# Kernel optimization log

Measured on AMD Instinct MI355X. Metric: run time of the kernel, lower is better.

Reference implementation:

```python
import jax, jax.numpy as jnp
import numpy as np

H, W, C, B = 64, 64, 512, 16

def _dwconv(x, w, b, k):
    # x: [B,C,H,W]; w: [C,1,k,k] depthwise kernel; b: [C]
    pad = k // 2
    out = jax.lax.conv_general_dilated(
        x, w, window_strides=(1, 1), padding=[(pad, pad), (pad, pad)],
        dimension_numbers=('NCHW', 'OIHW', 'NCHW'), feature_group_count=x.shape[1])
    return out + b[None, :, None, None]

def setup_inputs() -> dict:
    key = jax.random.key(0)
    ks = jax.random.split(key, 7)
    x = jax.random.normal(ks[0], (B, 1 + H * W, C), dtype=jnp.float32)
    def kinit(k, ksize):
        fan_in = ksize * ksize  # groups=C -> in_ch per group = 1
        bound = 1.0 / np.sqrt(fan_in)
        return jax.random.uniform(k, (C, 1, ksize, ksize), jnp.float32, -bound, bound)
    w7 = kinit(ks[1], 7); b7 = jax.random.uniform(ks[2], (C,), jnp.float32, -1/7.0, 1/7.0)
    w5 = kinit(ks[3], 5); b5 = jax.random.uniform(ks[4], (C,), jnp.float32, -1/5.0, 1/5.0)
    w3 = kinit(ks[5], 3); b3 = jax.random.uniform(ks[6], (C,), jnp.float32, -1/3.0, 1/3.0)
    return {'x': x, 'w7': w7, 'b7': b7, 'w5': w5, 'b5': b5, 'w3': w3, 'b3': b3}

def reference(x, w7, b7, w5, b5, w3, b3):
    Bn, N, Cn = x.shape
    cls_token = x[:, 0]          # [B, C]
    feat_token = x[:, 1:]        # [B, H*W, C]
    cnn_feat = feat_token.transpose(0, 2, 1).reshape(Bn, Cn, H, W)
    y = (_dwconv(cnn_feat, w7, b7, 7) + cnn_feat
         + _dwconv(cnn_feat, w5, b5, 5)
         + _dwconv(cnn_feat, w3, b3, 3))
    y = y.reshape(Bn, Cn, H * W).transpose(0, 2, 1)   # [B, HW, C]
    return jnp.concatenate([cls_token[:, None, :], y], axis=1)
```

## Files before the change

kernel.cpp:

```cpp
#include <hip/hip_runtime.h>

#define Hh 64
#define Ww 64
#define Cc 512
#define Bb 16
#define NTOK (1 + Hh * Ww)
#define TW 8
#define TH 4

typedef float v2f __attribute__((ext_vector_type(2)));

__global__ void ppeg_prep(const float* __restrict__ w7, const float* __restrict__ b7,
                          const float* __restrict__ w5, const float* __restrict__ b5,
                          const float* __restrict__ w3, const float* __restrict__ b3,
                          const float* __restrict__ x, float* __restrict__ wt,
                          float* __restrict__ beff, float* __restrict__ out) {
    int idx = blockIdx.x * blockDim.x + threadIdx.x;
    if (idx < Cc * 49) {
        int c = idx / 49, t = idx % 49;
        int r = t / 7, s = t % 7;
        float v = w7[idx];
        if (r >= 1 && r <= 5 && s >= 1 && s <= 5) v += w5[c * 25 + (r - 1) * 5 + (s - 1)];
        if (r >= 2 && r <= 4 && s >= 2 && s <= 4) v += w3[c * 9 + (r - 2) * 3 + (s - 2)];
        if (t == 24) v += 1.0f;
        wt[t * Cc + c] = v;
    }
    if (idx < Cc) beff[idx] = b7[idx] + b5[idx] + b3[idx];
    if (idx < Bb * Cc) {
        int b = idx / Cc, c = idx % Cc;
        size_t o = (size_t)b * NTOK * Cc + c;
        out[o] = x[o];
    }
}

__global__ __launch_bounds__(256, 2)
void ppeg_conv(const float* __restrict__ x, const float* __restrict__ wt,
               const float* __restrict__ beff, float* __restrict__ out) {
    const int tx = threadIdx.x;
    const int ty = threadIdx.y;

    const int L     = blockIdx.x + 32 * (blockIdx.y + 4 * blockIdx.z);
    const int g_lin = (L & 7) * 256 + (L >> 3);
    const int sp    = g_lin & 31;
    const int g     = g_lin >> 5;
    const int cb    = (g & 3) * 128;
    const int b     = g >> 2;

    const int c0 = cb + 2 * tx;
    const int wblk = sp & 7;
    const int hblk = sp >> 3;
    const int oh0   = hblk * (TH * 4) + ty * TH;
    const int wbase = wblk * TW;

    __shared__ float taps[49][128];
    const int tid = ty * 64 + tx;
    for (int idx = tid; idx < 49 * 128; idx += 256) {
        const int t = idx >> 7, ch = idx & 127;
        taps[t][ch] = wt[t * Cc + cb + ch];
    }
    __syncthreads();

    const float* xb = x + ((size_t)b * NTOK + 1) * Cc + c0;

    const v2f bias = *(const v2f*)&beff[c0];
    v2f acc[TH][TW];
#pragma unroll
    for (int o = 0; o < TH; ++o)
#pragma unroll
        for (int j = 0; j < TW; ++j) acc[o][j] = bias;

    const bool interior = (wblk != 0) && (wblk != 7);

#pragma unroll
    for (int k = 0; k < TH + 6; ++k) {
        const int ir = oh0 + k - 3;
        if (ir >= 0 && ir < Hh) {
            const float* xrow = xb + (size_t)ir * (Ww * Cc);
            v2f v[TW + 6];
            if (interior) {
#pragma unroll
                for (int j = 0; j < TW + 6; ++j)
                    v[j] = *(const v2f*)(xrow + (size_t)(wbase - 3 + j) * Cc);
            } else {
#pragma unroll
                for (int j = 0; j < TW + 6; ++j) {
                    const int wc = wbase + j - 3;
                    if (wc >= 0 && wc < Ww)
                        v[j] = *(const v2f*)(xrow + (size_t)wc * Cc);
                    else {
                        v[j].x = 0.0f; v[j].y = 0.0f;
                    }
                }
            }
#pragma unroll
            for (int o = 0; o < TH; ++o) {
                if (o > k || o < k - 6) continue;
                const int r = k - o;
#pragma unroll
                for (int s = 0; s < 7; ++s) {
                    const v2f tp = *(const v2f*)&taps[r * 7 + s][2 * tx];
#pragma unroll
                    for (int j = 0; j < TW; ++j) {
                        acc[o][j].x = fmaf(tp.x, v[j + s].x, acc[o][j].x);
                        acc[o][j].y = fmaf(tp.y, v[j + s].y, acc[o][j].y);
                    }
                }
            }
        }
    }

#pragma unroll
    for (int o = 0; o < TH; ++o) {
        float* orow = out + ((size_t)b * NTOK + 1 + (size_t)(oh0 + o) * Ww + wbase) * Cc + c0;
#pragma unroll
        for (int j = 0; j < TW; ++j)
            __builtin_nontemporal_store(acc[o][j], (v2f*)(orow + (size_t)j * Cc));
    }
}

extern "C" void kernel_launch(void* const* d_in, const int* in_sizes, int n_in,
                              void* d_out, int out_size, void* d_ws, size_t ws_size,
                              hipStream_t stream) {
    const float* x  = (const float*)d_in[0];
    const float* w7 = (const float*)d_in[1];
    const float* b7 = (const float*)d_in[2];
    const float* w5 = (const float*)d_in[3];
    const float* b5 = (const float*)d_in[4];
    const float* w3 = (const float*)d_in[5];
    const float* b3 = (const float*)d_in[6];
    float* out = (float*)d_out;

    float* wt   = (float*)d_ws;
    float* beff = wt + 49 * Cc;

    ppeg_prep<<<(Cc * 49 + 255) / 256, 256, 0, stream>>>(w7, b7, w5, b5, w3, b3,
                                                         x, wt, beff, out);

    dim3 grid(32, Cc / 128, Bb);
    dim3 block(64, 4);
    ppeg_conv<<<grid, block, 0, stream>>>(x, wt, beff, out);
}
```

Before: 271.1 us.

## Stage input rows through double-buffered LDS with async global_load_lds

Input rows are no longer read straight from global memory into each thread's registers. All four warps now share rows staged into a double-buffered LDS ring with the global_load_lds builtin, and output rows are interleaved across warps (row = 4*o + ty) so each staged row serves several warps. This removes redundant global/L2 reads of the overlapping halo rows and overlaps the fetch of the next rows with compute. The cost is a __syncthreads on every one of 22 row iterations, and the loop is fully unrolled, which risks serialization. Edge columns are clamped on load and then zeroed in registers.

```diff
diff --git a/kernel.cpp b/kernel.cpp
--- a/kernel.cpp
+++ b/kernel.cpp
@@ -6,9 +6,11 @@
 #define Bb 16
 #define NTOK (1 + Hh * Ww)
 #define TW 8
-#define TH 4
+#define NROWS 22
 
 typedef float v2f __attribute__((ext_vector_type(2)));
+typedef const float __attribute__((address_space(1))) gcf;
+typedef float       __attribute__((address_space(3))) lsf;
 
 __global__ void ppeg_prep(const float* __restrict__ w7, const float* __restrict__ b7,
                           const float* __restrict__ w5, const float* __restrict__ b5,
@@ -46,72 +48,92 @@
     const int cb    = (g & 3) * 128;
     const int b     = g >> 2;
 
-    const int c0 = cb + 2 * tx;
-    const int wblk = sp & 7;
-    const int hblk = sp >> 3;
-    const int oh0   = hblk * (TH * 4) + ty * TH;
+    const int wblk  = sp & 7;
+    const int hblk  = sp >> 3;
     const int wbase = wblk * TW;
+    const int ohb   = hblk * 16;
 
     __shared__ float taps[49][128];
+    __shared__ float rbuf[2][14][128];
+
     const int tid = ty * 64 + tx;
     for (int idx = tid; idx < 49 * 128; idx += 256) {
-        const int t = idx >> 7, ch = idx & 127;
-        taps[t][ch] = wt[t * Cc + cb + ch];
+        taps[idx >> 7][idx & 127] = wt[(idx >> 7) * Cc + cb + (idx & 127)];
     }
+
+    auto stage = [&](int m, int bufi) {
+        const int ir = ohb + m - 3;
+        if (ir < 0 || ir >= Hh) return;
+#pragma unroll
+        for (int tt = 0; tt < 2; ++tt) {
+            const int t = ty + 4 * tt;
+            if (t < 7) {
+                int pc = wbase - 3 + 2 * t + (tx >> 5);
+                pc = pc < 0 ? 0 : (pc > Ww - 1 ? Ww - 1 : pc);
+                const float* gp = x + ((size_t)b * NTOK + 1 + (size_t)ir * Ww + pc) * Cc
+                                    + cb + (tx & 31) * 4;
+                __builtin_amdgcn_global_load_lds((gcf*)gp, (lsf*)&rbuf[bufi][2 * t][0],
+                                                 16, 0, 0);
+            }
+        }
+    };
+
+    stage(0, 0);
+    stage(1, 1);
     __syncthreads();
 
-    const float* xb = x + ((size_t)b * NTOK + 1) * Cc + c0;
-
+    const int c0 = cb + 2 * tx;
     const v2f bias = *(const v2f*)&beff[c0];
-    v2f acc[TH][TW];
+    v2f acc[4][TW];
 #pragma unroll
-    for (int o = 0; o < TH; ++o)
+    for (int o = 0; o < 4; ++o)
 #pragma unroll
         for (int j = 0; j < TW; ++j) acc[o][j] = bias;
 
     const bool interior = (wblk != 0) && (wblk != 7);
 
 #pragma unroll
-    for (int k = 0; k < TH + 6; ++k) {
-        const int ir = oh0 + k - 3;
+    for (int m = 0; m < NROWS; ++m) {
+        const int ir = ohb + m - 3;
         if (ir >= 0 && ir < Hh) {
-            const float* xrow = xb + (size_t)ir * (Ww * Cc);
-            v2f v[TW + 6];
-            if (interior) {
+            const int d = m - ty;
+            if (d >= 0 && d <= 18) {
+                v2f v[14];
 #pragma unroll
-                for (int j = 0; j < TW + 6; ++j)
-                    v[j] = *(const v2f*)(xrow + (size_t)(wbase - 3 + j) * Cc);
-            } else {
+                for (int j = 0; j < 14; ++j)
+                    v[j] = *(const v2f*)&rbuf[m & 1][j][2 * tx];
+                if (!interior) {
 #pragma unroll
-                for (int j = 0; j < TW + 6; ++j) {
-                    const int wc = wbase + j - 3;
-                    if (wc >= 0 && wc < Ww)
-                        v[j] = *(const v2f*)(xrow + (size_t)wc * Cc);
-                    else {
-                        v[j].x = 0.0f; v[j].y = 0.0f;
+                    for (int j = 0; j < 14; ++j) {
+                        const int wc = wbase + j - 3;
+                        if (wc < 0 || wc >= Ww) { v[j].x = 0.0f; v[j].y = 0.0f; }
                     }
                 }
-            }
 #pragma unroll
-            for (int o = 0; o < TH; ++o) {
-                if (o > k || o < k - 6) continue;
-                const int r = k - o;
+                for (int o = 0; o < 4; ++o) {
+                    const int r = d - 4 * o;
+                    if (r >= 0 && r <= 6) {
 #pragma unroll
-                for (int s = 0; s < 7; ++s) {
-                    const v2f tp = *(const v2f*)&taps[r * 7 + s][2 * tx];
+                        for (int s = 0; s < 7; ++s) {
+                            const v2f tp = *(const v2f*)&taps[r * 7 + s][2 * tx];
 #pragma unroll
-                    for (int j = 0; j < TW; ++j) {
-                        acc[o][j].x = fmaf(tp.x, v[j + s].x, acc[o][j].x);
-                        acc[o][j].y = fmaf(tp.y, v[j + s].y, acc[o][j].y);
+                            for (int j = 0; j < TW; ++j) {
+                                acc[o][j].x = fmaf(tp.x, v[j + s].x, acc[o][j].x);
+                                acc[o][j].y = fmaf(tp.y, v[j + s].y, acc[o][j].y);
+                            }
+                        }
                     }
                 }
             }
         }
+        __syncthreads();
+        if (m + 2 < NROWS) stage(m + 2, m & 1);
     }
 
 #pragma unroll
-    for (int o = 0; o < TH; ++o) {
-        float* orow = out + ((size_t)b * NTOK + 1 + (size_t)(oh0 + o) * Ww + wbase) * Cc + c0;
+    for (int o = 0; o < 4; ++o) {
+        const int ohr = ohb + 4 * o + ty;
+        float* orow = out + ((size_t)b * NTOK + 1 + (size_t)ohr * Ww + wbase) * Cc + c0;
 #pragma unroll
         for (int j = 0; j < TW; ++j)
             __builtin_nontemporal_store(acc[o][j], (v2f*)(orow + (size_t)j * Cc));
```

New measurement: 289.1 us. 6.6% more time.
